# Kernel tuning notes

Measured on AMD Instinct MI355X. Metric: run time of the kernel, lower is better.

Reference implementation:

```python
import jax, jax.numpy as jnp
import numpy as np

EMB_DIM = 128
DEC_DIM = 128
NEG_INF = -1e10


def setup_inputs() -> dict:
    key = jax.random.key(0)
    k1, k2, k3, k4, k5, k6 = jax.random.split(key, 6)
    B, S = 64, 4096
    hidden = jax.random.normal(k1, (B, DEC_DIM), dtype=jnp.float32)
    seq_embs = jax.random.normal(k2, (S, B, EMB_DIM), dtype=jnp.float32)
    mask = jax.random.randint(k3, (B, S), 0, 2, dtype=jnp.int32)
    # nn.Linear(emb_dim + dec_dim, dec_dim): weight [dec_dim, emb_dim+dec_dim]
    fan_in = EMB_DIM + DEC_DIM
    bound = 1.0 / np.sqrt(fan_in)
    W_attn = jax.random.uniform(k4, (DEC_DIM, fan_in), minval=-bound, maxval=bound, dtype=jnp.float32)
    b_attn = jax.random.uniform(k5, (DEC_DIM,), minval=-bound, maxval=bound, dtype=jnp.float32)
    # nn.Linear(dec_dim, 1, bias=False): weight [1, dec_dim]
    bound_v = 1.0 / np.sqrt(DEC_DIM)
    v_w = jax.random.uniform(k6, (1, DEC_DIM), minval=-bound_v, maxval=bound_v, dtype=jnp.float32)
    return {"hidden": hidden, "seq_embs": seq_embs, "mask": mask,
            "W_attn": W_attn, "b_attn": b_attn, "v_w": v_w}


def reference(hidden, seq_embs, mask, W_attn, b_attn, v_w):
    # hidden: [B, Dd]; seq_embs: [S, B, De]; mask: [B, S]
    # Concat order in torch is (hidden, seq_embs) -> split W accordingly.
    Wh = W_attn[:, :DEC_DIM]   # [Dd, Dd] applied to hidden
    We = W_attn[:, DEC_DIM:]   # [Dd, De] applied to seq_embs
    embs = jnp.transpose(seq_embs, (1, 0, 2))            # [B, S, De]
    # energy = tanh(Linear(cat(hidden, embs))) without materializing concat
    h_proj = hidden @ Wh.T + b_attn                       # [B, Dd]
    e_proj = jnp.einsum('bse,de->bsd', embs, We)          # [B, S, Dd]
    energy = jnp.tanh(h_proj[:, None, :] + e_proj)        # [B, S, Dd]
    attention = jnp.einsum('bsd,d->bs', energy, v_w[0])   # [B, S]
    attention = jnp.where(mask == 0, NEG_INF, attention)
    return jax.nn.softmax(attention, axis=1)
```

## Files before the change

### kernel.cpp

```cpp
#include <hip/hip_runtime.h>
#include <hip/hip_bf16.h>

#define BB 64
#define SS 4096
#define EE 128
#define DD 128
#define FAN 256
#define TILES 4
#define NEG_INF_F (-1e10f)

typedef __bf16 bf16x8 __attribute__((ext_vector_type(8)));
typedef unsigned short u16x8 __attribute__((ext_vector_type(8)));
typedef float f32x4 __attribute__((ext_vector_type(4)));

__device__ inline bf16x8 ld_frag(const unsigned short* p) {
    union { u16x8 u; bf16x8 b; } c;
    c.u = *(const u16x8*)p;
    return c.b;
}

__device__ inline uint2 f4_to_bf4(float4 f) {
    union { __hip_bfloat162 b; unsigned u; } lo, hi;
    lo.b = __float22bfloat162_rn(make_float2(f.x, f.y));
    hi.b = __float22bfloat162_rn(make_float2(f.z, f.w));
    return make_uint2(lo.u, hi.u);
}

__device__ inline float tanh_fast(float x) {
    float ax = fabsf(x);
    float e = __expf(-2.0f * ax);
    float t = (1.0f - e) * __builtin_amdgcn_rcpf(1.0f + e);
    return x < 0.0f ? -t : t;
}

__global__ __launch_bounds__(256) void prep_kernel(
        const float* __restrict__ hidden, const float* __restrict__ W_attn,
        const float* __restrict__ b_attn, const float* __restrict__ v_w,
        float* __restrict__ hproj, unsigned short* __restrict__ Wb,
        float* __restrict__ v_out) {
    const int b = blockIdx.x;
    const int t = threadIdx.x;
    if (t < 128) {
        float acc = b_attn[t];
        const float4* hrow = (const float4*)(hidden + b * DD);
        const float4* wrow = (const float4*)(W_attn + t * FAN);
        #pragma unroll
        for (int e = 0; e < 32; e++) {
            float4 h = hrow[e], w = wrow[e];
            acc += h.x * w.x + h.y * w.y + h.z * w.z + h.w * w.w;
        }
        hproj[b * DD + t] = acc;
        if (b == 0) v_out[t] = v_w[t];
    } else {
        int tt = t - 128;
        int d  = 2 * b + (tt >> 6);
        int e0 = (tt & 63) * 2;
        float2 src = *(const float2*)(W_attn + d * FAN + DD + e0);
        union { __hip_bfloat162 bb; unsigned u; } c;
        c.bb = __float22bfloat162_rn(src);
        *(unsigned*)&Wb[d * EE + e0] = c.u;
    }
}

__global__ __launch_bounds__(256, 4) void logits_kernel(
        const float* __restrict__ seq_embs, const int* __restrict__ mask,
        const float* __restrict__ hproj, const unsigned short* __restrict__ Wb,
        const float* __restrict__ v, float* __restrict__ logits) {
    __shared__ __attribute__((aligned(16))) unsigned short Ws[128][136];

    const int b    = blockIdx.y;
    const int g    = blockIdx.x;
    const int tid  = threadIdx.x;
    const int wave = tid >> 6;
    const int lane = tid & 63;
    const int m    = lane & 15;
    const int quad = lane >> 4;

    const int arow = wave * 16 + m;

    const int* __restrict__ mask_g = mask + (size_t)b * SS + g * (TILES * 64);
    const float* __restrict__ xbase = seq_embs
        + (size_t)(g * (TILES * 64) + arow) * (BB * EE)
        + (size_t)b * EE + quad * 8;

    const uint4* __restrict__ Wb16 = (const uint4*)Wb;
    uint4 wstage[8];
    #pragma unroll
    for (int k = 0; k < 8; k++) wstage[k] = Wb16[tid + k * 256];
    #pragma unroll
    for (int k = 0; k < 8; k++) {
        const int i = tid + k * 256;
        *(uint4*)&Ws[i >> 4][(i & 15) * 8] = wstage[k];
    }

    int am[2];
    int4 mq[2];
    bf16x8 af[2][4];
    {
        am[0] = mask_g[arow];
        mq[0] = *(const int4*)(mask_g + wave * 16 + quad * 4);
        const float* xrow = xbase;
        #pragma unroll
        for (int kk = 0; kk < 4; kk++) {
            union { uint4 q; bf16x8 bf; } c;
            c.q = make_uint4(0u, 0u, 0u, 0u);
            if (am[0] != 0) {
                float4 f0 = *(const float4*)(xrow + kk * 32);
                float4 f1 = *(const float4*)(xrow + kk * 32 + 4);
                uint2 a = f4_to_bf4(f0), bq = f4_to_bf4(f1);
                c.q = make_uint4(a.x, a.y, bq.x, bq.y);
            }
            af[0][kk] = c.bf;
        }
    }
    __syncthreads();

    float hp_r[8], v_r[8];
    #pragma unroll
    for (int t = 0; t < 8; t++) {
        hp_r[t] = hproj[b * DD + t * 16 + m];
        v_r[t]  = v[t * 16 + m];
    }

    #pragma unroll
    for (int tile = 0; tile < TILES; tile++) {
        const int cur = tile & 1;
        if (tile + 1 < TILES) {
            const int nxt = cur ^ 1;
            am[nxt] = mask_g[(tile + 1) * 64 + arow];
            mq[nxt] = *(const int4*)(mask_g + (tile + 1) * 64 + wave * 16 + quad * 4);
            const float* xrow = xbase + (size_t)((tile + 1) * 64) * (BB * EE);
            #pragma unroll
            for (int kk = 0; kk < 4; kk++) {
                union { uint4 q; bf16x8 bf; } c;
                c.q = make_uint4(0u, 0u, 0u, 0u);
                if (am[nxt] != 0) {
                    float4 f0 = *(const float4*)(xrow + kk * 32);
                    float4 f1 = *(const float4*)(xrow + kk * 32 + 4);
                    uint2 a = f4_to_bf4(f0), bq = f4_to_bf4(f1);
                    c.q = make_uint4(a.x, a.y, bq.x, bq.y);
                }
                af[nxt][kk] = c.bf;
            }
        }

        f32x4 acc[8];
        #pragma unroll
        for (int t = 0; t < 8; t++) acc[t] = (f32x4){0.f, 0.f, 0.f, 0.f};
        #pragma unroll
        for (int kk = 0; kk < 4; kk++) {
            const int k0 = kk * 32 + quad * 8;
            #pragma unroll
            for (int t = 0; t < 8; t++) {
                bf16x8 bf = ld_frag(&Ws[t * 16 + m][k0]);
                acc[t] = __builtin_amdgcn_mfma_f32_16x16x32_bf16(af[cur][kk], bf, acc[t], 0, 0, 0);
            }
        }

        const int mqa[4] = {mq[cur].x, mq[cur].y, mq[cur].z, mq[cur].w};
        float red[4];
        #pragma unroll
        for (int r = 0; r < 4; r++) {
            float part = 0.f;
            if (mqa[r] != 0) {
                #pragma unroll
                for (int t = 0; t < 8; t++)
                    part += v_r[t] * tanh_fast(hp_r[t] + acc[t][r]);
                part += __shfl_xor(part, 1);
                part += __shfl_xor(part, 2);
                part += __shfl_xor(part, 4);
                part += __shfl_xor(part, 8);
            }
            red[r] = (mqa[r] != 0) ? part : NEG_INF_F;
        }
        if (m == 0) {
            float4 o = make_float4(red[0], red[1], red[2], red[3]);
            *(float4*)&logits[(size_t)b * SS + g * (TILES * 64) + tile * 64
                              + wave * 16 + quad * 4] = o;
        }
    }
}

__global__ __launch_bounds__(256) void softmax_kernel(float* __restrict__ logits) {
    const int b = blockIdx.x;
    const int tid = threadIdx.x;
    const int wave = tid >> 6;
    const int lane = tid & 63;
    float* row = logits + (size_t)b * SS;

    float4 vals[4];
    float lmax = -1e30f;
    #pragma unroll
    for (int i = 0; i < 4; i++) {
        vals[i] = *(const float4*)(row + (size_t)(i * 256 + tid) * 4);
        lmax = fmaxf(lmax, fmaxf(fmaxf(vals[i].x, vals[i].y), fmaxf(vals[i].z, vals[i].w)));
    }
    #pragma unroll
    for (int off = 32; off >= 1; off >>= 1)
        lmax = fmaxf(lmax, __shfl_xor(lmax, off));

    __shared__ float smax[4], ssum[4];
    if (lane == 0) smax[wave] = lmax;
    __syncthreads();
    const float gmax = fmaxf(fmaxf(smax[0], smax[1]), fmaxf(smax[2], smax[3]));

    float lsum = 0.f;
    #pragma unroll
    for (int i = 0; i < 4; i++) {
        vals[i].x = __expf(vals[i].x - gmax);
        vals[i].y = __expf(vals[i].y - gmax);
        vals[i].z = __expf(vals[i].z - gmax);
        vals[i].w = __expf(vals[i].w - gmax);
        lsum += (vals[i].x + vals[i].y) + (vals[i].z + vals[i].w);
    }
    #pragma unroll
    for (int off = 32; off >= 1; off >>= 1)
        lsum += __shfl_xor(lsum, off);
    if (lane == 0) ssum[wave] = lsum;
    __syncthreads();
    const float total = (ssum[0] + ssum[1]) + (ssum[2] + ssum[3]);
    const float inv = 1.0f / total;

    #pragma unroll
    for (int i = 0; i < 4; i++) {
        float4 o;
        o.x = vals[i].x * inv; o.y = vals[i].y * inv;
        o.z = vals[i].z * inv; o.w = vals[i].w * inv;
        *(float4*)(row + (size_t)(i * 256 + tid) * 4) = o;
    }
}

extern "C" void kernel_launch(void* const* d_in, const int* in_sizes, int n_in,
                              void* d_out, int out_size, void* d_ws, size_t ws_size,
                              hipStream_t stream) {
    const float* hidden   = (const float*)d_in[0];
    const float* seq_embs = (const float*)d_in[1];
    const int*   mask     = (const int*)d_in[2];
    const float* W_attn   = (const float*)d_in[3];
    const float* b_attn   = (const float*)d_in[4];
    const float* v_w      = (const float*)d_in[5];
    float* out = (float*)d_out;

    float*          hproj = (float*)d_ws;
    unsigned short* Wb    = (unsigned short*)((char*)d_ws + 32768);
    float*          vv    = (float*)((char*)d_ws + 65536);

    prep_kernel<<<64, 256, 0, stream>>>(hidden, W_attn, b_attn, v_w, hproj, Wb, vv);
    dim3 grid(SS / (64 * TILES), BB);
    logits_kernel<<<grid, 256, 0, stream>>>(seq_embs, mask, hproj, Wb, vv, out);
    softmax_kernel<<<BB, 256, 0, stream>>>(out);
}
```

Before: 211.6 us.

## Fuse exp into logits kernel with atomic row sums, swizzled LDS weights via direct loads

The logits kernel now applies exp directly and accumulates per-row sums with atomics, so a light normalization kernel replaces the max/sum softmax pass. The max subtraction is dropped, which relies on logits staying small enough not to overflow exp. Weights are pre-swizzled in prep and loaded straight into LDS with global_load_lds to cut staging registers and bank conflicts. Tiles per block drop from 4 to 2, each B fragment is reused across both tiles, and all activation loads are issued up front instead of double-buffered.

```diff
diff --git a/kernel.cpp b/kernel.cpp
--- a/kernel.cpp
+++ b/kernel.cpp
@@ -6,14 +6,15 @@
 #define EE 128
 #define DD 128
 #define FAN 256
-#define TILES 4
+#define TILES 2
+#define ROWS (TILES * 64)
 #define NEG_INF_F (-1e10f)
 
 typedef __bf16 bf16x8 __attribute__((ext_vector_type(8)));
 typedef unsigned short u16x8 __attribute__((ext_vector_type(8)));
 typedef float f32x4 __attribute__((ext_vector_type(4)));
 
-__device__ inline bf16x8 ld_frag(const unsigned short* p) {
+__device__ inline bf16x8 ld_frag_lds(const unsigned char* p) {
     union { u16x8 u; bf16x8 b; } c;
     c.u = *(const u16x8*)p;
     return c.b;
@@ -36,10 +37,11 @@
 __global__ __launch_bounds__(256) void prep_kernel(
         const float* __restrict__ hidden, const float* __restrict__ W_attn,
         const float* __restrict__ b_attn, const float* __restrict__ v_w,
-        float* __restrict__ hproj, unsigned short* __restrict__ Wb,
-        float* __restrict__ v_out) {
+        float* __restrict__ hproj, unsigned char* __restrict__ Wb,
+        float* __restrict__ v_out, float* __restrict__ sums) {
     const int b = blockIdx.x;
     const int t = threadIdx.x;
+    if (t == 0) sums[b] = 0.0f;
     if (t < 128) {
         float acc = b_attn[t];
         const float4* hrow = (const float4*)(hidden + b * DD);
@@ -58,15 +60,18 @@
         float2 src = *(const float2*)(W_attn + d * FAN + DD + e0);
         union { __hip_bfloat162 bb; unsigned u; } c;
         c.bb = __float22bfloat162_rn(src);
-        *(unsigned*)&Wb[d * EE + e0] = c.u;
+        unsigned off = (unsigned)(d * 256)
+                     + (((unsigned)(e0 * 2)) ^ (((unsigned)d & 7u) << 4));
+        *(unsigned*)(Wb + off) = c.u;
     }
 }
 
 __global__ __launch_bounds__(256, 4) void logits_kernel(
         const float* __restrict__ seq_embs, const int* __restrict__ mask,
-        const float* __restrict__ hproj, const unsigned short* __restrict__ Wb,
-        const float* __restrict__ v, float* __restrict__ logits) {
-    __shared__ __attribute__((aligned(16))) unsigned short Ws[128][136];
+        const float* __restrict__ hproj, const unsigned char* __restrict__ Wb,
+        const float* __restrict__ v, float* __restrict__ out,
+        float* __restrict__ sums) {
+    __shared__ __attribute__((aligned(1024))) unsigned char Ws[DD * EE * 2];
 
     const int b    = blockIdx.y;
     const int g    = blockIdx.x;
@@ -76,44 +81,40 @@
     const int m    = lane & 15;
     const int quad = lane >> 4;
 
-    const int arow = wave * 16 + m;
-
-    const int* __restrict__ mask_g = mask + (size_t)b * SS + g * (TILES * 64);
-    const float* __restrict__ xbase = seq_embs
-        + (size_t)(g * (TILES * 64) + arow) * (BB * EE)
+    #pragma unroll
+    for (int j = 0; j < 8; j++) {
+        const int c = wave * 8 + j;
+        __builtin_amdgcn_global_load_lds(
+            (const __attribute__((address_space(1))) unsigned int*)(Wb + c * 1024 + lane * 16),
+            (__attribute__((address_space(3))) unsigned int*)(Ws + c * 1024),
+            16, 0, 0);
+    }
+
+    const int* __restrict__ mask_g = mask + (size_t)b * SS + g * ROWS;
+    int  am[TILES];
+    int4 mq[TILES];
+    bf16x8 af[TILES][4];
+    const float* __restrict__ xb = seq_embs
+        + (size_t)(g * ROWS + wave * 16 + m) * (BB * EE)
         + (size_t)b * EE + quad * 8;
-
-    const uint4* __restrict__ Wb16 = (const uint4*)Wb;
-    uint4 wstage[8];
-    #pragma unroll
-    for (int k = 0; k < 8; k++) wstage[k] = Wb16[tid + k * 256];
-    #pragma unroll
-    for (int k = 0; k < 8; k++) {
-        const int i = tid + k * 256;
-        *(uint4*)&Ws[i >> 4][(i & 15) * 8] = wstage[k];
-    }
-
-    int am[2];
-    int4 mq[2];
-    bf16x8 af[2][4];
-    {
-        am[0] = mask_g[arow];
-        mq[0] = *(const int4*)(mask_g + wave * 16 + quad * 4);
-        const float* xrow = xbase;
+    #pragma unroll
+    for (int tl = 0; tl < TILES; tl++) {
+        am[tl] = mask_g[tl * 64 + wave * 16 + m];
+        mq[tl] = *(const int4*)(mask_g + tl * 64 + wave * 16 + quad * 4);
+        const float* xr = xb + (size_t)(tl * 64) * (BB * EE);
         #pragma unroll
         for (int kk = 0; kk < 4; kk++) {
-            union { uint4 q; bf16x8 bf; } c;
-            c.q = make_uint4(0u, 0u, 0u, 0u);
-            if (am[0] != 0) {
-                float4 f0 = *(const float4*)(xrow + kk * 32);
-                float4 f1 = *(const float4*)(xrow + kk * 32 + 4);
+            union { uint4 q; bf16x8 bf; } cc;
+            cc.q = make_uint4(0u, 0u, 0u, 0u);
+            if (am[tl] != 0) {
+                float4 f0 = *(const float4*)(xr + kk * 32);
+                float4 f1 = *(const float4*)(xr + kk * 32 + 4);
                 uint2 a = f4_to_bf4(f0), bq = f4_to_bf4(f1);
-                c.q = make_uint4(a.x, a.y, bq.x, bq.y);
+                cc.q = make_uint4(a.x, a.y, bq.x, bq.y);
             }
-            af[0][kk] = c.bf;
-        }
-    }
-    __syncthreads();
+            af[tl][kk] = cc.bf;
+        }
+    }
 
     float hp_r[8], v_r[8];
     #pragma unroll
@@ -122,112 +123,69 @@
         v_r[t]  = v[t * 16 + m];
     }
 
-    #pragma unroll
-    for (int tile = 0; tile < TILES; tile++) {
-        const int cur = tile & 1;
-        if (tile + 1 < TILES) {
-            const int nxt = cur ^ 1;
-            am[nxt] = mask_g[(tile + 1) * 64 + arow];
-            mq[nxt] = *(const int4*)(mask_g + (tile + 1) * 64 + wave * 16 + quad * 4);
-            const float* xrow = xbase + (size_t)((tile + 1) * 64) * (BB * EE);
+    __syncthreads();
+
+    float part[TILES][4];
+    #pragma unroll
+    for (int tl = 0; tl < TILES; tl++)
+        #pragma unroll
+        for (int r = 0; r < 4; r++) part[tl][r] = 0.0f;
+
+    const unsigned sw = ((unsigned)(m & 7)) << 4;
+    #pragma unroll
+    for (int t = 0; t < 8; t++) {
+        const unsigned rbase = (unsigned)((t * 16 + m) * 256);
+        bf16x8 bf[4];
+        #pragma unroll
+        for (int kk = 0; kk < 4; kk++) {
+            const unsigned cb = ((unsigned)(kk * 64 + quad * 16)) ^ sw;
+            bf[kk] = ld_frag_lds(Ws + rbase + cb);
+        }
+        #pragma unroll
+        for (int tl = 0; tl < TILES; tl++) {
+            f32x4 acc = (f32x4){0.f, 0.f, 0.f, 0.f};
             #pragma unroll
-            for (int kk = 0; kk < 4; kk++) {
-                union { uint4 q; bf16x8 bf; } c;
-                c.q = make_uint4(0u, 0u, 0u, 0u);
-                if (am[nxt] != 0) {
-                    float4 f0 = *(const float4*)(xrow + kk * 32);
-                    float4 f1 = *(const float4*)(xrow + kk * 32 + 4);
-                    uint2 a = f4_to_bf4(f0), bq = f4_to_bf4(f1);
-                    c.q = make_uint4(a.x, a.y, bq.x, bq.y);
-                }
-                af[nxt][kk] = c.bf;
-            }
-        }
-
-        f32x4 acc[8];
-        #pragma unroll
-        for (int t = 0; t < 8; t++) acc[t] = (f32x4){0.f, 0.f, 0.f, 0.f};
-        #pragma unroll
-        for (int kk = 0; kk < 4; kk++) {
-            const int k0 = kk * 32 + quad * 8;
+            for (int kk = 0; kk < 4; kk++)
+                acc = __builtin_amdgcn_mfma_f32_16x16x32_bf16(af[tl][kk], bf[kk], acc, 0, 0, 0);
             #pragma unroll
-            for (int t = 0; t < 8; t++) {
-                bf16x8 bf = ld_frag(&Ws[t * 16 + m][k0]);
-                acc[t] = __builtin_amdgcn_mfma_f32_16x16x32_bf16(af[cur][kk], bf, acc[t], 0, 0, 0);
-            }
-        }
-
-        const int mqa[4] = {mq[cur].x, mq[cur].y, mq[cur].z, mq[cur].w};
+            for (int r = 0; r < 4; r++)
+                part[tl][r] += v_r[t] * tanh_fast(hp_r[t] + acc[r]);
+        }
+    }
+
+    float blocksum = 0.0f;
+    #pragma unroll
+    for (int tl = 0; tl < TILES; tl++) {
+        const int mqa[4] = {mq[tl].x, mq[tl].y, mq[tl].z, mq[tl].w};
         float red[4];
         #pragma unroll
         for (int r = 0; r < 4; r++) {
-            float part = 0.f;
-            if (mqa[r] != 0) {
-                #pragma unroll
-                for (int t = 0; t < 8; t++)
-                    part += v_r[t] * tanh_fast(hp_r[t] + acc[t][r]);
-                part += __shfl_xor(part, 1);
-                part += __shfl_xor(part, 2);
-                part += __shfl_xor(part, 4);
-                part += __shfl_xor(part, 8);
-            }
-            red[r] = (mqa[r] != 0) ? part : NEG_INF_F;
+            float p = part[tl][r];
+            p += __shfl_xor(p, 1);
+            p += __shfl_xor(p, 2);
+            p += __shfl_xor(p, 4);
+            p += __shfl_xor(p, 8);
+            red[r] = (mqa[r] != 0) ? __expf(p) : 0.0f;
+            blocksum += red[r];
         }
         if (m == 0) {
-            float4 o = make_float4(red[0], red[1], red[2], red[3]);
-            *(float4*)&logits[(size_t)b * SS + g * (TILES * 64) + tile * 64
-                              + wave * 16 + quad * 4] = o;
-        }
-    }
-}
-
-__global__ __launch_bounds__(256) void softmax_kernel(float* __restrict__ logits) {
-    const int b = blockIdx.x;
-    const int tid = threadIdx.x;
-    const int wave = tid >> 6;
-    const int lane = tid & 63;
-    float* row = logits + (size_t)b * SS;
-
-    float4 vals[4];
-    float lmax = -1e30f;
-    #pragma unroll
-    for (int i = 0; i < 4; i++) {
-        vals[i] = *(const float4*)(row + (size_t)(i * 256 + tid) * 4);
-        lmax = fmaxf(lmax, fmaxf(fmaxf(vals[i].x, vals[i].y), fmaxf(vals[i].z, vals[i].w)));
-    }
-    #pragma unroll
-    for (int off = 32; off >= 1; off >>= 1)
-        lmax = fmaxf(lmax, __shfl_xor(lmax, off));
-
-    __shared__ float smax[4], ssum[4];
-    if (lane == 0) smax[wave] = lmax;
-    __syncthreads();
-    const float gmax = fmaxf(fmaxf(smax[0], smax[1]), fmaxf(smax[2], smax[3]));
-
-    float lsum = 0.f;
-    #pragma unroll
-    for (int i = 0; i < 4; i++) {
-        vals[i].x = __expf(vals[i].x - gmax);
-        vals[i].y = __expf(vals[i].y - gmax);
-        vals[i].z = __expf(vals[i].z - gmax);
-        vals[i].w = __expf(vals[i].w - gmax);
-        lsum += (vals[i].x + vals[i].y) + (vals[i].z + vals[i].w);
-    }
-    #pragma unroll
-    for (int off = 32; off >= 1; off >>= 1)
-        lsum += __shfl_xor(lsum, off);
-    if (lane == 0) ssum[wave] = lsum;
-    __syncthreads();
-    const float total = (ssum[0] + ssum[1]) + (ssum[2] + ssum[3]);
-    const float inv = 1.0f / total;
-
-    #pragma unroll
-    for (int i = 0; i < 4; i++) {
-        float4 o;
-        o.x = vals[i].x * inv; o.y = vals[i].y * inv;
-        o.z = vals[i].z * inv; o.w = vals[i].w * inv;
-        *(float4*)(row + (size_t)(i * 256 + tid) * 4) = o;
-    }
+            *(float4*)&out[(size_t)b * SS + g * ROWS + tl * 64 + wave * 16 + quad * 4] =
+                make_float4(red[0], red[1], red[2], red[3]);
+        }
+    }
+    blocksum += __shfl_xor(blocksum, 16);
+    blocksum += __shfl_xor(blocksum, 32);
+    if (lane == 0) atomicAdd(&sums[b], blocksum);
+}
+
+__global__ __launch_bounds__(256) void norm_kernel(
+        float* __restrict__ out, const float* __restrict__ sums) {
+    const int b = blockIdx.y;
+    const float inv = 1.0f / sums[b];
+    const int i = (blockIdx.x * 256 + threadIdx.x) * 4;
+    float4 v = *(float4*)&out[(size_t)b * SS + i];
+    v.x *= inv; v.y *= inv; v.z *= inv; v.w *= inv;
+    *(float4*)&out[(size_t)b * SS + i] = v;
 }
 
 extern "C" void kernel_launch(void* const* d_in, const int* in_sizes, int n_in,
@@ -241,12 +199,14 @@
     const float* v_w      = (const float*)d_in[5];
     float* out = (float*)d_out;
 
-    float*          hproj = (float*)d_ws;
-    unsigned short* Wb    = (unsigned short*)((char*)d_ws + 32768);
-    float*          vv    = (float*)((char*)d_ws + 65536);
-
-    prep_kernel<<<64, 256, 0, stream>>>(hidden, W_attn, b_attn, v_w, hproj, Wb, vv);
-    dim3 grid(SS / (64 * TILES), BB);
-    logits_kernel<<<grid, 256, 0, stream>>>(seq_embs, mask, hproj, Wb, vv, out);
-    softmax_kernel<<<BB, 256, 0, stream>>>(out);
-}
+    float*         hproj = (float*)d_ws;
+    unsigned char* Wb    = (unsigned char*)d_ws + 32768;
+    float*         vv    = (float*)((char*)d_ws + 65536);
+    float*         sums  = (float*)((char*)d_ws + 66048);
+
+    prep_kernel<<<64, 256, 0, stream>>>(hidden, W_attn, b_attn, v_w, hproj, Wb, vv, sums);
+    dim3 grid(SS / ROWS, BB);
+    logits_kernel<<<grid, 256, 0, stream>>>(seq_embs, mask, hproj, Wb, vv, out, sums);
+    dim3 ngrid(SS / (256 * 4), BB);
+    norm_kernel<<<ngrid, 256, 0, stream>>>(out, sums);
+}
```

New measurement: 261.6 us. 1.24x slower.
